# Kernel optimization log

Measured on AMD Instinct MI355X. Metric: run time of the kernel, lower is better.

## Reference

```python
import jax, jax.numpy as jnp
import numpy as np

TEMPERATURE = 0.07
EPS = 1e-8


def setup_inputs() -> dict:
    key = jax.random.key(0)
    k1, k2 = jax.random.split(key)
    N, D, NUM_CLASSES = 8192, 512, 512
    embeddings = jax.random.normal(k1, (N, D), dtype=jnp.float32)
    labels = jax.random.randint(k2, (N,), 0, NUM_CLASSES, dtype=jnp.int64)
    return {"embeddings": embeddings, "labels": labels}


def reference(embeddings, labels):
    N = embeddings.shape[0]
    # L2 normalize rows
    e = embeddings / jnp.linalg.norm(embeddings, axis=1, keepdims=True)
    sim = jnp.matmul(e, e.T) / TEMPERATURE  # [N, N]
    pos_mask = (labels[:, None] == labels[None, :])
    pos_mask = pos_mask & ~jnp.eye(N, dtype=bool)  # zero diagonal
    # original: pos_sims = sim * pos_mask; keep only pos_sims > 0
    valid_pos = pos_mask & (sim > 0)
    exp_sim = jnp.exp(sim)
    numerator = jnp.sum(jnp.where(valid_pos, exp_sim, 0.0), axis=1)  # [N]
    denominator = exp_sim.sum(axis=1) - jnp.diagonal(exp_sim)        # [N]
    row_valid = jnp.any(valid_pos, axis=1) & (denominator > 0)
    # guard against log(0) on invalid rows
    num_safe = jnp.where(row_valid, numerator, 1.0)
    den_safe = jnp.where(row_valid, denominator, 1.0)
    loss_i = -jnp.log(num_safe / (den_safe + EPS))
    n_valid = jnp.sum(row_valid)
    mean_loss = jnp.sum(jnp.where(row_valid, loss_i, 0.0)) / jnp.maximum(n_valid, 1)
    loss = jnp.where(n_valid > 0, mean_loss, 0.0)
    return jnp.abs(loss)
```

## Files before the change

kernel.cpp:

```cpp
#include <hip/hip_runtime.h>

#define INV_T (1.0f / 0.07f)
#define EPSF 1e-8f

typedef float f32x4 __attribute__((ext_vector_type(4)));
typedef long longx2 __attribute__((ext_vector_type(2)));
typedef int i32x8 __attribute__((ext_vector_type(8)));

struct TrueT { static constexpr bool value = true; };
struct FalseT { static constexpr bool value = false; };

union frag_u { longx2 h[2]; i32x8 v; };

__global__ __launch_bounds__(256) void norm_kernel(const float* __restrict__ emb,
                                                   unsigned char* __restrict__ e8,
                                                   float* __restrict__ num,
                                                   float* __restrict__ den,
                                                   float* __restrict__ acc2,
                                                   int D) {
  const int wave = threadIdx.x >> 6;
  const int lane = threadIdx.x & 63;
  const int row = blockIdx.x * 4 + wave;
  const float4* src = (const float4*)(emb + (size_t)row * D);
  float4 v0 = src[lane];
  float4 v1 = src[lane + 64];
  float ss = v0.x * v0.x + v0.y * v0.y + v0.z * v0.z + v0.w * v0.w +
             v1.x * v1.x + v1.y * v1.y + v1.z * v1.z + v1.w * v1.w;
#pragma unroll
  for (int m = 32; m >= 1; m >>= 1) ss += __shfl_xor(ss, m, 64);
  const float r = 1.0f / sqrtf(ss);
  int w0 = __builtin_amdgcn_cvt_pk_fp8_f32(v0.x * r, v0.y * r, 0, false);
  w0 = __builtin_amdgcn_cvt_pk_fp8_f32(v0.z * r, v0.w * r, w0, true);
  int w1 = __builtin_amdgcn_cvt_pk_fp8_f32(v1.x * r, v1.y * r, 0, false);
  w1 = __builtin_amdgcn_cvt_pk_fp8_f32(v1.z * r, v1.w * r, w1, true);
  unsigned int* dst = (unsigned int*)(e8 + (size_t)row * D);
  dst[lane] = (unsigned int)w0;
  dst[64 + lane] = (unsigned int)w1;
  if (lane == 0) { num[row] = 0.f; den[row] = 0.f; }
  if (blockIdx.x == 0 && threadIdx.x < 2) acc2[threadIdx.x] = 0.f;
}

template <int D, int KT>
__global__ __launch_bounds__(256, 3) void sim_kernel(
    const unsigned char* __restrict__ E,
    const int* __restrict__ labels,
    float* __restrict__ num, float* __restrict__ den) {
  __shared__ __align__(16) char smem[40960];
  float* red = (float*)smem;

  const int tid = threadIdx.x;
  const int lane = tid & 63;
  const int wave = tid >> 6;
  const int wm = wave >> 1, wn = wave & 1;
  const int fr = lane & 15;
  const int fk = lane >> 4;

  const int bid = blockIdx.x;
  const int t = (bid & 7) * 260 + (bid >> 3);
  int bb = (int)((sqrtf(8.0f * (float)t + 1.0f) - 1.0f) * 0.5f);
  while ((bb + 1) * (bb + 2) / 2 <= t) ++bb;
  while (bb * (bb + 1) / 2 > t) --bb;
  const int ba = t - bb * (bb + 1) / 2;
  const int i0 = ba * 128;
  const int j0 = bb * 128;
  const bool diag = (i0 == j0);

  f32x4 acc[4][4] = {};

  const int sw = (fr & 7) << 4;
  const int c0 = (fk * 32) ^ sw;
  const int c1 = (fk * 32 + 16) ^ sw;
  const int abase = (wm * 64 + fr) * 128;
  const int bbase = 16384 + (wn * 64 + fr) * 128;

  const int srow = tid >> 1;
  const int shalf = (tid & 1) * 64;
  const unsigned char* gA = E + (size_t)(i0 + srow) * D + shalf;
  const unsigned char* gB = E + (size_t)(j0 + srow) * D + shalf;
  const int ssw = (srow & 7) << 4;
  const int wbase = srow * 128;

  longx2 P[8];

  auto loadR = [&](int st) {
    const int kb = st * 128;
#pragma unroll
    for (int u = 0; u < 4; ++u) {
      P[u] = *(const longx2*)(gA + kb + u * 16);
      P[4 + u] = *(const longx2*)(gB + kb + u * 16);
    }
  };

  auto dsW = [&]() {
#pragma unroll
    for (int u = 0; u < 4; ++u) {
      *(longx2*)(smem + wbase + ((shalf + u * 16) ^ ssw)) = P[u];
      *(longx2*)(smem + 16384 + wbase + ((shalf + u * 16) ^ ssw)) = P[4 + u];
    }
  };

  auto compute = [&]() {
    frag_u A[4], B[4];
#pragma unroll
    for (int m = 0; m < 4; ++m) {
      A[m].h[0] = *(const longx2*)(smem + abase + m * 2048 + c0);
      A[m].h[1] = *(const longx2*)(smem + abase + m * 2048 + c1);
    }
#pragma unroll
    for (int n = 0; n < 4; ++n) {
      B[n].h[0] = *(const longx2*)(smem + bbase + n * 2048 + c0);
      B[n].h[1] = *(const longx2*)(smem + bbase + n * 2048 + c1);
    }
    __builtin_amdgcn_s_setprio(1);
#pragma unroll
    for (int m = 0; m < 4; ++m)
#pragma unroll
      for (int n = 0; n < 4; ++n)
        acc[m][n] = __builtin_amdgcn_mfma_scale_f32_16x16x128_f8f6f4(
            A[m].v, B[n].v, acc[m][n], 0, 0,
            0, 0x7F7F7F7F, 0, 0x7F7F7F7F);
    __builtin_amdgcn_s_setprio(0);
  };

#define BARRIER_SEQ                                           \
  asm volatile("s_waitcnt lgkmcnt(0)" ::: "memory");          \
  __builtin_amdgcn_sched_barrier(0);                          \
  __builtin_amdgcn_s_barrier();                               \
  __builtin_amdgcn_sched_barrier(0);

  loadR(0);
  dsW();
  BARRIER_SEQ;

#pragma unroll
  for (int st = 0; st < KT; ++st) {
    if (st + 1 < KT) loadR(st + 1);
    compute();
    if (st + 1 < KT) {
      __builtin_amdgcn_s_barrier();
      __builtin_amdgcn_sched_barrier(0);
      dsW();
      BARRIER_SEQ;
    }
  }
  __syncthreads();

  int jcol[4], labj[4];
#pragma unroll
  for (int n = 0; n < 4; ++n) {
    jcol[n] = j0 + wn * 64 + n * 16 + fr;
    labj[n] = labels[jcol[n]];
  }
  float cd[4] = {0.f, 0.f, 0.f, 0.f}, cn[4] = {0.f, 0.f, 0.f, 0.f};

  auto epilogue = [&](auto DIAG) {
#pragma unroll
    for (int m = 0; m < 4; ++m) {
      float pdm[4] = {0.f, 0.f, 0.f, 0.f}, pnm[4] = {0.f, 0.f, 0.f, 0.f};
      const int ibase = i0 + wm * 64 + m * 16 + fk * 4;
      int li[4];
#pragma unroll
      for (int r = 0; r < 4; ++r) li[r] = labels[ibase + r];
#pragma unroll
      for (int n = 0; n < 4; ++n) {
#pragma unroll
        for (int r = 0; r < 4; ++r) {
          const float s = acc[m][n][r] * INV_T;
          const float es = __expf(s);
          if (DIAG.value) {
            if (jcol[n] != ibase + r) {
              pdm[r] += es;
              if (li[r] == labj[n] && s > 0.0f) pnm[r] += es;
            }
          } else {
            pdm[r] += es;
            cd[n] += es;
            if (li[r] == labj[n] && s > 0.0f) { pnm[r] += es; cn[n] += es; }
          }
        }
      }
      const int base = ((wave * 4 + m) * 64 + (lane ^ (m << 2))) * 5;
#pragma unroll
      for (int r = 0; r < 4; ++r) {
        red[base + r] = pdm[r];
        red[5120 + base + r] = pnm[r];
      }
    }
  };

  if (diag) epilogue(TrueT{}); else epilogue(FalseT{});

  if (!diag) {
#pragma unroll
    for (int sh = 16; sh < 64; sh <<= 1) {
#pragma unroll
      for (int n = 0; n < 4; ++n) {
        cd[n] += __shfl_xor(cd[n], sh, 64);
        cn[n] += __shfl_xor(cn[n], sh, 64);
      }
    }
    if (fk == 0) {
#pragma unroll
      for (int n = 0; n < 4; ++n) {
        atomicAdd(&den[jcol[n]], cd[n]);
        atomicAdd(&num[jcol[n]], cn[n]);
      }
    }
  }

  __syncthreads();
  {
    const int which = tid >> 7;
    const int ri = tid & 127;
    const int cwm = ri >> 6, cm = (ri >> 4) & 3, cfk = (ri >> 2) & 3, cr = ri & 3;
    const float* src = red + which * 5120;
    float v = 0.f;
#pragma unroll
    for (int w2 = 0; w2 < 2; ++w2)
#pragma unroll
      for (int f2 = 0; f2 < 16; ++f2)
        v += src[(((cwm * 2 + w2) * 4 + cm) * 64 + ((cfk * 16 + f2) ^ (cm << 2))) * 5 + cr];
    atomicAdd((which ? num : den) + i0 + ri, v);
  }
}

__global__ __launch_bounds__(256) void loss_reduce(const float* __restrict__ num,
                                                   const float* __restrict__ den,
                                                   float* __restrict__ acc2, int N) {
  const int tid = threadIdx.x;
  int i = blockIdx.x * 512 + tid;
  float sum = 0.f, cnt = 0.f;
#pragma unroll
  for (int k = 0; k < 2; ++k, i += 256) {
    const float n = num[i], d = den[i];
    if (n > 0.f && d > 0.f) {
      sum += logf(d + EPSF) - logf(n);
      cnt += 1.f;
    }
  }
#pragma unroll
  for (int m = 32; m >= 1; m >>= 1) {
    sum += __shfl_xor(sum, m, 64);
    cnt += __shfl_xor(cnt, m, 64);
  }
  __shared__ float s1[4], s2[4];
  if ((tid & 63) == 0) { s1[tid >> 6] = sum; s2[tid >> 6] = cnt; }
  __syncthreads();
  if (tid == 0) {
    atomicAdd(&acc2[0], s1[0] + s1[1] + s1[2] + s1[3]);
    atomicAdd(&acc2[1], s2[0] + s2[1] + s2[2] + s2[3]);
  }
}

__global__ void final_kernel(const float* __restrict__ acc2, float* __restrict__ out) {
  const float S = acc2[0], C = acc2[1];
  out[0] = (C > 0.f) ? fabsf(S / C) : 0.f;
}

extern "C" void kernel_launch(void* const* d_in, const int* in_sizes, int n_in,
                              void* d_out, int out_size, void* d_ws, size_t ws_size,
                              hipStream_t stream) {
  const float* emb = (const float*)d_in[0];
  const int* labels = (const int*)d_in[1];
  float* out = (float*)d_out;

  const int N = in_sizes[1];
  const int D = in_sizes[0] / N;

  unsigned char* e8 = (unsigned char*)d_ws;
  float* num = (float*)((char*)d_ws + (size_t)N * D);
  float* den = num + N;
  float* acc2 = den + N;

  norm_kernel<<<N / 4, 256, 0, stream>>>(emb, e8, num, den, acc2, D);
  const int nb = N / 128;
  const int tri = nb * (nb + 1) / 2;
  sim_kernel<512, 4><<<tri, 256, 0, stream>>>(e8, labels, num, den);
  loss_reduce<<<N / 512, 256, 0, stream>>>(num, den, acc2, N);
  final_kernel<<<1, 1, 0, stream>>>(acc2, out);
}
```

Measured before the change: 62.23 us.

## Double-buffer LDS tiles with two-stage register prefetch in sim kernel

Doubles the shared-memory tile buffer to 64KB and uses two register staging sets so global loads run two K-steps ahead while compute reads the alternate LDS buffer. This removes one barrier per K-step, since writes go to the buffer not being read. B fragments are now loaded per column inside the MFMA loop to reduce register pressure. Occupancy bound drops from 3 to 2 blocks per CU because of the larger LDS use and extra registers, which may reduce latency hiding.

```diff
diff --git a/kernel.cpp b/kernel.cpp
--- a/kernel.cpp
+++ b/kernel.cpp
@@ -41,11 +41,11 @@
 }
 
 template <int D, int KT>
-__global__ __launch_bounds__(256, 3) void sim_kernel(
+__global__ __launch_bounds__(256, 2) void sim_kernel(
     const unsigned char* __restrict__ E,
     const int* __restrict__ labels,
     float* __restrict__ num, float* __restrict__ den) {
-  __shared__ __align__(16) char smem[40960];
+  __shared__ __align__(16) char smem[65536];
   float* red = (float*)smem;
 
   const int tid = threadIdx.x;
@@ -80,9 +80,9 @@
   const int ssw = (srow & 7) << 4;
   const int wbase = srow * 128;
 
-  longx2 P[8];
-
-  auto loadR = [&](int st) {
+  longx2 Pa[8], Pb[8];
+
+  auto loadR = [&](int st, longx2 (&P)[8]) {
     const int kb = st * 128;
 #pragma unroll
     for (int u = 0; u < 4; ++u) {
@@ -91,34 +91,36 @@
     }
   };
 
-  auto dsW = [&]() {
+  auto dsW = [&](int buf, const longx2 (&P)[8]) {
+    char* base = smem + buf * 32768;
 #pragma unroll
     for (int u = 0; u < 4; ++u) {
-      *(longx2*)(smem + wbase + ((shalf + u * 16) ^ ssw)) = P[u];
-      *(longx2*)(smem + 16384 + wbase + ((shalf + u * 16) ^ ssw)) = P[4 + u];
-    }
-  };
-
-  auto compute = [&]() {
-    frag_u A[4], B[4];
+      *(longx2*)(base + wbase + ((shalf + u * 16) ^ ssw)) = P[u];
+      *(longx2*)(base + 16384 + wbase + ((shalf + u * 16) ^ ssw)) = P[4 + u];
+    }
+  };
+
+  auto compute = [&](int buf) {
+    const char* Ab = smem + buf * 32768 + abase;
+    const char* Bb = smem + buf * 32768 + bbase;
+    frag_u A[4];
 #pragma unroll
     for (int m = 0; m < 4; ++m) {
-      A[m].h[0] = *(const longx2*)(smem + abase + m * 2048 + c0);
-      A[m].h[1] = *(const longx2*)(smem + abase + m * 2048 + c1);
-    }
+      A[m].h[0] = *(const longx2*)(Ab + m * 2048 + c0);
+      A[m].h[1] = *(const longx2*)(Ab + m * 2048 + c1);
+    }
+    __builtin_amdgcn_s_setprio(1);
 #pragma unroll
     for (int n = 0; n < 4; ++n) {
-      B[n].h[0] = *(const longx2*)(smem + bbase + n * 2048 + c0);
-      B[n].h[1] = *(const longx2*)(smem + bbase + n * 2048 + c1);
-    }
-    __builtin_amdgcn_s_setprio(1);
-#pragma unroll
-    for (int m = 0; m < 4; ++m)
-#pragma unroll
-      for (int n = 0; n < 4; ++n)
+      frag_u Bn;
+      Bn.h[0] = *(const longx2*)(Bb + n * 2048 + c0);
+      Bn.h[1] = *(const longx2*)(Bb + n * 2048 + c1);
+#pragma unroll
+      for (int m = 0; m < 4; ++m)
         acc[m][n] = __builtin_amdgcn_mfma_scale_f32_16x16x128_f8f6f4(
-            A[m].v, B[n].v, acc[m][n], 0, 0,
+            A[m].v, Bn.v, acc[m][n], 0, 0,
             0, 0x7F7F7F7F, 0, 0x7F7F7F7F);
+    }
     __builtin_amdgcn_s_setprio(0);
   };
 
@@ -128,19 +130,21 @@
   __builtin_amdgcn_s_barrier();                               \
   __builtin_amdgcn_sched_barrier(0);
 
-  loadR(0);
-  dsW();
+  loadR(0, Pa);
+  dsW(0, Pa);
+  loadR(1, Pb);
   BARRIER_SEQ;
 
 #pragma unroll
   for (int st = 0; st < KT; ++st) {
-    if (st + 1 < KT) loadR(st + 1);
-    compute();
-    if (st + 1 < KT) {
-      __builtin_amdgcn_s_barrier();
-      __builtin_amdgcn_sched_barrier(0);
-      dsW();
-      BARRIER_SEQ;
+    if (st & 1) {
+      if (st + 2 < KT) loadR(st + 2, Pb);
+      compute(1);
+      if (st + 1 < KT) { dsW(0, Pa); BARRIER_SEQ; }
+    } else {
+      if (st + 2 < KT) loadR(st + 2, Pa);
+      compute(0);
+      if (st + 1 < KT) { dsW(1, Pb); BARRIER_SEQ; }
     }
   }
   __syncthreads();
```

New measurement: 57.78 us. -7.1%, faster.
